# Kernel tuning notes

Hardware: AMD Instinct MI355X
Metric: run time of the kernel (lower is better)

## Reference

```python
import jax, jax.numpy as jnp
import numpy as np

B, P, E = 16, 1024, 768
HID, HEADS = 768, 12
DH = HID // HEADS  # 64
EPS = 1e-5


def setup_inputs() -> dict:
    key = jax.random.key(0)
    ks = jax.random.split(key, 4)
    return {
        "x": jax.random.normal(ks[0], (B, P, E), dtype=jnp.float32),
        "ln_weight": jnp.ones((P, E), dtype=jnp.float32),
        "ln_bias": jnp.zeros((P, E), dtype=jnp.float32),
        "qkv": jax.random.normal(ks[1], (E, 3 * HID), dtype=jnp.float32),
        "lin_w": jax.random.normal(ks[2], (HID, E), dtype=jnp.float32) * 0.02,
        "lin_b": jax.random.normal(ks[3], (E,), dtype=jnp.float32) * 0.02,
    }


def reference(x, ln_weight, ln_bias, qkv, lin_w, lin_b):
    # LayerNorm over the last TWO dims (patches, emb), per torch nn.LayerNorm((P, E))
    mean = jnp.mean(x, axis=(-2, -1), keepdims=True)
    var = jnp.var(x, axis=(-2, -1), keepdims=True)
    xn = (x - mean) / jnp.sqrt(var + EPS) * ln_weight + ln_bias

    # QKV projection: [B,P,E] @ [E,3*HID] -> [B,P,3*HID]
    proj = xn @ qkv
    # view(B,P,heads,-1) then permute -> [B,heads,P,3*DH]; chunk along last dim
    proj = proj.reshape(B, P, HEADS, 3 * DH).transpose(0, 2, 1, 3)
    q, k, v = proj[..., :DH], proj[..., DH:2 * DH], proj[..., 2 * DH:]

    # Softmax-free attention: (Q K^T) V
    atten = jnp.einsum("bhqd,bhkd->bhqk", q, k)  # [B,H,P,P]
    out = jnp.einsum("bhqk,bhkd->bhqd", atten, v)  # [B,H,P,DH]

    out = out.transpose(0, 2, 1, 3).reshape(B, P, HID)
    # dropout p=0.0 (eval) -> identity
    out = jax.nn.relu(out @ lin_w + lin_b)
    return out + x
```

## Files before the change

kernel.cpp:

```cpp
#include <hip/hip_runtime.h>
#include <hip/hip_bf16.h>
#include <cstdint>

#define BB   16
#define PP   1024
#define EE   768
#define HID  768
#define NH   12
#define DH   64
#define NPB  (PP * EE)
#define MROWS (BB * PP)

typedef __bf16 bf16_t;
typedef __bf16 bf16x8 __attribute__((ext_vector_type(8)));
typedef float  f32x4  __attribute__((ext_vector_type(4)));

__device__ __forceinline__ void gld16(const void* g, void* l) {
    __builtin_amdgcn_global_load_lds(
        (const __attribute__((address_space(1))) void*)(uintptr_t)g,
        (__attribute__((address_space(3))) void*)(uint32_t)(uintptr_t)l,
        16, 0, 0);
}

__global__ __launch_bounds__(256) void stats1_kernel(const float* __restrict__ x,
                                                     float* __restrict__ part) {
    int bid = blockIdx.x;
    int b = bid >> 6, s = bid & 63;
    const float4* xp = (const float4*)(x + (size_t)b * NPB + (size_t)s * 12288);
    float sum = 0.f, ss = 0.f;
#pragma unroll
    for (int i = 0; i < 12; ++i) {
        float4 v = xp[i * 256 + threadIdx.x];
        sum += v.x + v.y + v.z + v.w;
        ss  += v.x * v.x + v.y * v.y + v.z * v.z + v.w * v.w;
    }
#pragma unroll
    for (int off = 32; off > 0; off >>= 1) {
        sum += __shfl_down(sum, off, 64);
        ss  += __shfl_down(ss,  off, 64);
    }
    __shared__ float tmp[8];
    int wave = threadIdx.x >> 6, lane = threadIdx.x & 63;
    if (lane == 0) { tmp[wave * 2] = sum; tmp[wave * 2 + 1] = ss; }
    __syncthreads();
    if (threadIdx.x == 0) {
        part[bid * 2]     = tmp[0] + tmp[2] + tmp[4] + tmp[6];
        part[bid * 2 + 1] = tmp[1] + tmp[3] + tmp[5] + tmp[7];
    }
}

__global__ __launch_bounds__(256) void prep_kernel(const float* __restrict__ qkvw,
                                                   const float* __restrict__ linw,
                                                   const float* __restrict__ part,
                                                   bf16_t* __restrict__ qkvT,
                                                   bf16_t* __restrict__ lwT,
                                                   float* __restrict__ stats) {
    int bid = blockIdx.x;
    if (bid < 6912) {
        int idx = bid * 256 + threadIdx.x;
        int c = idx / 768, r = idx - c * 768;
        qkvT[idx] = (bf16_t)qkvw[(size_t)r * 2304 + c];
    } else if (bid < 9216) {
        int idx = (bid - 6912) * 256 + threadIdx.x;
        int c = idx / 768, r = idx - c * 768;
        lwT[idx] = (bf16_t)linw[(size_t)r * 768 + c];
    } else {
        int wave = threadIdx.x >> 6, lane = threadIdx.x & 63;
#pragma unroll
        for (int j = 0; j < 4; ++j) {
            int b = wave * 4 + j;
            float sum = part[(b * 64 + lane) * 2];
            float ss  = part[(b * 64 + lane) * 2 + 1];
#pragma unroll
            for (int off = 32; off > 0; off >>= 1) {
                sum += __shfl_down(sum, off, 64);
                ss  += __shfl_down(ss,  off, 64);
            }
            if (lane == 0) {
                const float inv_n = 1.f / (float)NPB;
                float mean = sum * inv_n;
                float var  = ss * inv_n - mean * mean;
                stats[b * 2]     = mean;
                stats[b * 2 + 1] = rsqrtf(var + 1e-5f);
            }
        }
    }
}

__global__ __launch_bounds__(256) void ln_apply_kernel(const float* __restrict__ x,
                                                       const float* __restrict__ lnw,
                                                       const float* __restrict__ lnb,
                                                       const float* __restrict__ stats,
                                                       bf16_t* __restrict__ xn) {
    int i = (blockIdx.x * 256 + threadIdx.x) * 8;
    int b = i / NPB;
    int r = i - b * NPB;
    float mean = stats[b * 2], rstd = stats[b * 2 + 1];
    float4 x0 = *(const float4*)(x + i),     x1 = *(const float4*)(x + i + 4);
    float4 w0 = *(const float4*)(lnw + r),   w1 = *(const float4*)(lnw + r + 4);
    float4 c0 = *(const float4*)(lnb + r),   c1 = *(const float4*)(lnb + r + 4);
    union { bf16_t h[8]; uint4 u; } o;
    o.h[0] = (bf16_t)((x0.x - mean) * rstd * w0.x + c0.x);
    o.h[1] = (bf16_t)((x0.y - mean) * rstd * w0.y + c0.y);
    o.h[2] = (bf16_t)((x0.z - mean) * rstd * w0.z + c0.z);
    o.h[3] = (bf16_t)((x0.w - mean) * rstd * w0.w + c0.w);
    o.h[4] = (bf16_t)((x1.x - mean) * rstd * w1.x + c1.x);
    o.h[5] = (bf16_t)((x1.y - mean) * rstd * w1.y + c1.y);
    o.h[6] = (bf16_t)((x1.z - mean) * rstd * w1.z + c1.z);
    o.h[7] = (bf16_t)((x1.w - mean) * rstd * w1.w + c1.w);
    *(uint4*)(xn + i) = o.u;
}

template <int KDIM>
__device__ __forceinline__ void gemm_core_128(const bf16_t* __restrict__ A,
                                              const bf16_t* __restrict__ Bt,
                                              int mBase, int nBase,
                                              f32x4 acc[4][4],
                                              bf16_t* As, bf16_t* Bs) {
    const int t = threadIdx.x;
    const int lane = t & 63, wave = t >> 6;
    const int wm = wave >> 1, wn = wave & 1;
    const int m16 = lane & 15, quad = lane >> 4;

    const int sr = t >> 3, s8 = t & 7;
    const bf16_t* pa[4]; const bf16_t* pb[4];
#pragma unroll
    for (int i = 0; i < 4; ++i) {
        int row = i * 32 + sr;
        int g = (s8 - (row & 7)) & 7;
        pa[i] = A  + (size_t)(mBase + row) * KDIM + g * 8;
        pb[i] = Bt + (size_t)(nBase + row) * KDIM + g * 8;
    }

    int raOff[4][2], rbOff[4][2];
#pragma unroll
    for (int i = 0; i < 4; ++i) {
        int ra = wm * 64 + i * 16 + m16;
        int rb = wn * 64 + i * 16 + m16;
#pragma unroll
        for (int ks = 0; ks < 2; ++ks) {
            raOff[i][ks] = ra * 64 + (((ks * 4 + quad) + (ra & 7)) & 7) * 8;
            rbOff[i][ks] = rb * 64 + (((ks * 4 + quad) + (rb & 7)) & 7) * 8;
        }
    }

    const f32x4 z = {0.f, 0.f, 0.f, 0.f};
#pragma unroll
    for (int mm = 0; mm < 4; ++mm)
#pragma unroll
        for (int nn = 0; nn < 4; ++nn) acc[mm][nn] = z;

    for (int k0 = 0; k0 < KDIM; k0 += 64) {
        __syncthreads();
#pragma unroll
        for (int i = 0; i < 4; ++i) {
            gld16(pa[i] + k0, As + i * 2048 + t * 8);
            gld16(pb[i] + k0, Bs + i * 2048 + t * 8);
        }
        __syncthreads();
#pragma unroll
        for (int ks = 0; ks < 2; ++ks) {
            bf16x8 af[4], bfv[4];
#pragma unroll
            for (int i = 0; i < 4; ++i) {
                af[i]  = *(const bf16x8*)(As + raOff[i][ks]);
                bfv[i] = *(const bf16x8*)(Bs + rbOff[i][ks]);
            }
#pragma unroll
            for (int mm = 0; mm < 4; ++mm)
#pragma unroll
                for (int nn = 0; nn < 4; ++nn)
                    acc[mm][nn] = __builtin_amdgcn_mfma_f32_16x16x32_bf16(
                        af[mm], bfv[nn], acc[mm][nn], 0, 0, 0);
        }
    }
}

__global__ __launch_bounds__(256) void gemm_qkv_kernel(const bf16_t* __restrict__ xn,
                                                       const bf16_t* __restrict__ qkvT,
                                                       bf16_t* __restrict__ q,
                                                       bf16_t* __restrict__ kt,
                                                       bf16_t* __restrict__ vt) {
    __shared__ bf16_t smem[16384];
    f32x4 acc[4][4];
    const int lb  = blockIdx.y * 18 + blockIdx.x;
    const int swz = (lb & 7) * 288 + (lb >> 3);
    const int tx  = swz % 18, ty = swz / 18;
    const int mBase = ty * 128, nBase = tx * 128;
    gemm_core_128<768>(xn, qkvT, mBase, nBase, acc, smem, smem + 8192);

    const int t = threadIdx.x;
    const int lane = t & 63, wave = t >> 6;
    const int wm = wave >> 1, wn = wave & 1;
    const int m16 = lane & 15, quad = lane >> 4;
    const int b = mBase >> 10, p0 = mBase & 1023;

#pragma unroll
    for (int half = 0; half < 2; ++half) {
        const int g = tx * 2 + half;
        const int cls = g % 3, h = g / 3;
        const size_t bh = (size_t)(b * NH + h);
        __syncthreads();
        if (cls == 0) {
            if (wn == half) {
#pragma unroll
                for (int mm = 0; mm < 4; ++mm)
#pragma unroll
                    for (int nn = 0; nn < 4; ++nn)
#pragma unroll
                        for (int i = 0; i < 4; ++i)
                            smem[(wm * 64 + mm * 16 + quad * 4 + i) * 72 + nn * 16 + m16] =
                                (bf16_t)acc[mm][nn][i];
            }
            __syncthreads();
#pragma unroll
            for (int it = 0; it < 4; ++it) {
                int slot = it * 256 + t;
                int r = slot >> 3, cc = slot & 7;
                bf16x8 val = *(const bf16x8*)(smem + r * 72 + cc * 8);
                *(bf16x8*)(q + ((size_t)(b * PP + p0 + r)) * HID + h * DH + cc * 8) = val;
            }
        } else {
            bf16_t* dst = (cls == 1) ? kt : vt;
            if (wn == half) {
#pragma unroll
                for (int mm = 0; mm < 4; ++mm)
#pragma unroll
                    for (int nn = 0; nn < 4; ++nn) {
                        int c = nn * 16 + m16;
                        int r0 = wm * 64 + mm * 16 + quad * 4;
                        union { bf16_t hh[4]; uint2 u; } pk;
#pragma unroll
                        for (int i = 0; i < 4; ++i) pk.hh[i] = (bf16_t)acc[mm][nn][i];
                        *(uint2*)(&smem[c * 136 + r0]) = pk.u;
                    }
            }
            __syncthreads();
#pragma unroll
            for (int it = 0; it < 4; ++it) {
                int slot = it * 256 + t;
                int d = slot >> 4, pc = slot & 15;
                bf16x8 val = *(const bf16x8*)(smem + d * 136 + pc * 8);
                *(bf16x8*)(dst + (bh * DH + d) * PP + p0 + pc * 8) = val;
            }
        }
    }
}

__global__ __launch_bounds__(256) void kv_kernel(const bf16_t* __restrict__ kt,
                                                 const bf16_t* __restrict__ vt,
                                                 bf16_t* __restrict__ thi,
                                                 bf16_t* __restrict__ tlo) {
    __shared__ float red[4 * 64 * 65];
    const int bh = blockIdx.x;
    const bf16_t* Kb = kt + (size_t)bh * DH * PP;
    const bf16_t* Vb = vt + (size_t)bh * DH * PP;
    const int t = threadIdx.x;
    const int lane = t & 63, wave = t >> 6;
    const int m16 = lane & 15, quad = lane >> 4;
    const f32x4 z = {0.f, 0.f, 0.f, 0.f};
    f32x4 acc[4][4];
#pragma unroll
    for (int mm = 0; mm < 4; ++mm)
#pragma unroll
        for (int nn = 0; nn < 4; ++nn) acc[mm][nn] = z;

    for (int ks = 0; ks < 8; ++ks) {
        int kb = wave * 256 + ks * 32 + quad * 8;
        bf16x8 af[4], bfv[4];
#pragma unroll
        for (int mm = 0; mm < 4; ++mm)
            af[mm] = *(const bf16x8*)(Kb + (size_t)(mm * 16 + m16) * PP + kb);
#pragma unroll
        for (int nn = 0; nn < 4; ++nn)
            bfv[nn] = *(const bf16x8*)(Vb + (size_t)(nn * 16 + m16) * PP + kb);
#pragma unroll
        for (int mm = 0; mm < 4; ++mm)
#pragma unroll
            for (int nn = 0; nn < 4; ++nn)
                acc[mm][nn] = __builtin_amdgcn_mfma_f32_16x16x32_bf16(
                    af[mm], bfv[nn], acc[mm][nn], 0, 0, 0);
    }
#pragma unroll
    for (int mm = 0; mm < 4; ++mm)
#pragma unroll
        for (int nn = 0; nn < 4; ++nn)
#pragma unroll
            for (int i = 0; i < 4; ++i)
                red[wave * 4160 + (mm * 16 + quad * 4 + i) * 65 + nn * 16 + m16] =
                    acc[mm][nn][i];
    __syncthreads();
#pragma unroll
    for (int j = 0; j < 16; ++j) {
        int idx = j * 256 + t;
        int m = idx >> 6, n = idx & 63;
        int a = m * 65 + n;
        float s = red[a] + red[4160 + a] + red[8320 + a] + red[12480 + a];
        bf16_t hi = (bf16_t)s;
        float lo = s - (float)hi;
        thi[(size_t)bh * 4096 + idx] = hi;
        tlo[(size_t)bh * 4096 + idx] = (bf16_t)lo;
    }
}

__global__ __launch_bounds__(256) void u_kernel(const bf16_t* __restrict__ thi,
                                                const bf16_t* __restrict__ tlo,
                                                const bf16_t* __restrict__ lwT,
                                                bf16_t* __restrict__ ut) {
    const int bh = blockIdx.x;
    const int b = bh / NH, h = bh - b * NH;
    const int nBase = blockIdx.y * 256;
    const bf16_t* Th = thi + (size_t)bh * 4096;
    const bf16_t* Tl = tlo + (size_t)bh * 4096;
    const int t = threadIdx.x, lane = t & 63, wave = t >> 6;
    const int wm = wave >> 1, wn = wave & 1;
    const int m16 = lane & 15, quad = lane >> 4;
    const f32x4 z = {0.f, 0.f, 0.f, 0.f};
    f32x4 acc[2][8];
#pragma unroll
    for (int mm = 0; mm < 2; ++mm)
#pragma unroll
        for (int nn = 0; nn < 8; ++nn) acc[mm][nn] = z;

#pragma unroll
    for (int ks = 0; ks < 2; ++ks) {
        bf16x8 ah[2], al[2], bfr[8];
#pragma unroll
        for (int mm = 0; mm < 2; ++mm) {
            ah[mm] = *(const bf16x8*)(Th + (wm * 32 + mm * 16 + m16) * 64 + ks * 32 + quad * 8);
            al[mm] = *(const bf16x8*)(Tl + (wm * 32 + mm * 16 + m16) * 64 + ks * 32 + quad * 8);
        }
#pragma unroll
        for (int nn = 0; nn < 8; ++nn)
            bfr[nn] = *(const bf16x8*)(
                lwT + (size_t)(nBase + wn * 128 + nn * 16 + m16) * 768 + h * 64 + ks * 32 + quad * 8);
#pragma unroll
        for (int mm = 0; mm < 2; ++mm)
#pragma unroll
            for (int nn = 0; nn < 8; ++nn) {
                acc[mm][nn] = __builtin_amdgcn_mfma_f32_16x16x32_bf16(
                    ah[mm], bfr[nn], acc[mm][nn], 0, 0, 0);
                acc[mm][nn] = __builtin_amdgcn_mfma_f32_16x16x32_bf16(
                    al[mm], bfr[nn], acc[mm][nn], 0, 0, 0);
            }
    }
#pragma unroll
    for (int mm = 0; mm < 2; ++mm)
#pragma unroll
        for (int nn = 0; nn < 8; ++nn) {
            int e  = nBase + wn * 128 + nn * 16 + m16;
            int d1 = wm * 32 + mm * 16 + quad * 4;
            union { bf16_t hh[4]; uint2 u; } pk;
#pragma unroll
            for (int i = 0; i < 4; ++i) pk.hh[i] = (bf16_t)acc[mm][nn][i];
            *(uint2*)(ut + ((size_t)b * 768 + e) * 768 + h * 64 + d1) = pk.u;
        }
}

__global__ __launch_bounds__(256) void gemm_out_kernel(const bf16_t* __restrict__ q,
                                                       const bf16_t* __restrict__ ut,
                                                       const float* __restrict__ linb,
                                                       const float* __restrict__ x,
                                                       float* __restrict__ out) {
    __shared__ bf16_t smem[16384];
    f32x4 acc[4][4];
    const int lb  = blockIdx.y * 6 + blockIdx.x;
    const int swz = (lb & 7) * 96 + (lb >> 3);
    const int tx  = swz % 6, ty = swz / 6;
    const int mBase = ty * 128, nBase = tx * 128;
    const int b = mBase >> 10;
    gemm_core_128<768>(q, ut + (size_t)b * 768 * 768, mBase, nBase, acc,
                       smem, smem + 8192);

    const int lane = threadIdx.x & 63, wave = threadIdx.x >> 6;
    const int wm = wave >> 1, wn = wave & 1;
    const int m16 = lane & 15, quad = lane >> 4;
#pragma unroll
    for (int mm = 0; mm < 4; ++mm) {
#pragma unroll
        for (int i = 0; i < 4; ++i) {
            size_t row = mBase + wm * 64 + mm * 16 + quad * 4 + i;
#pragma unroll
            for (int nn = 0; nn < 4; ++nn) {
                int col = nBase + wn * 64 + nn * 16 + m16;
                float v = acc[mm][nn][i] + linb[col];
                v = fmaxf(v, 0.f) + x[row * EE + col];
                out[row * EE + col] = v;
            }
        }
    }
}

extern "C" void kernel_launch(void* const* d_in, const int* in_sizes, int n_in,
                              void* d_out, int out_size, void* d_ws, size_t ws_size,
                              hipStream_t stream) {
    const float* x    = (const float*)d_in[0];
    const float* lnw  = (const float*)d_in[1];
    const float* lnb  = (const float*)d_in[2];
    const float* qkvw = (const float*)d_in[3];
    const float* linw = (const float*)d_in[4];
    const float* linb = (const float*)d_in[5];
    float* out = (float*)d_out;
    char* ws = (char*)d_ws;

    float*  part  = (float*)(ws + 0);
    float*  stats = (float*)(ws + 8192);
    bf16_t* xn    = (bf16_t*)(ws + 8448);
    bf16_t* qkvT  = (bf16_t*)(ws + 25174272);
    bf16_t* lwT   = (bf16_t*)(ws + 28713216);
    bf16_t* q     = (bf16_t*)(ws + 29892864);
    bf16_t* kt    = (bf16_t*)(ws + 55058688);
    bf16_t* vt    = (bf16_t*)(ws + 80224512);
    bf16_t* thi   = qkvT;
    bf16_t* tlo   = qkvT + 192 * 4096;
    bf16_t* ut    = kt;

    stats1_kernel<<<dim3(BB * 64), dim3(256), 0, stream>>>(x, part);
    prep_kernel<<<dim3(9217), dim3(256), 0, stream>>>(qkvw, linw, part, qkvT, lwT, stats);
    ln_apply_kernel<<<dim3(6144), dim3(256), 0, stream>>>(x, lnw, lnb, stats, xn);
    gemm_qkv_kernel<<<dim3(18, 128), dim3(256), 0, stream>>>(xn, qkvT, q, kt, vt);
    kv_kernel<<<dim3(192), dim3(256), 0, stream>>>(kt, vt, thi, tlo);
    u_kernel<<<dim3(192, 3), dim3(256), 0, stream>>>(thi, tlo, lwT, ut);
    gemm_out_kernel<<<dim3(6, 128), dim3(256), 0, stream>>>(q, ut, linb, x, out);
}
```

Baseline: 276.6 us.

## Enlarge QKV GEMM to 256x256 tiles with double-buffered LDS and tiled weight transpose

```diff
diff --git a/kernel.cpp b/kernel.cpp
--- a/kernel.cpp
+++ b/kernel.cpp
@@ -56,14 +56,37 @@
                                                    bf16_t* __restrict__ lwT,
                                                    float* __restrict__ stats) {
     int bid = blockIdx.x;
-    if (bid < 6912) {
-        int idx = bid * 256 + threadIdx.x;
-        int c = idx / 768, r = idx - c * 768;
-        qkvT[idx] = (bf16_t)qkvw[(size_t)r * 2304 + c];
-    } else if (bid < 9216) {
-        int idx = (bid - 6912) * 256 + threadIdx.x;
-        int c = idx / 768, r = idx - c * 768;
-        lwT[idx] = (bf16_t)linw[(size_t)r * 768 + c];
+    if (bid < 576) {
+        __shared__ float lds[64][65];
+        const float* src; bf16_t* dst; int r0, c0, W;
+        if (bid < 432) {
+            int tr = bid / 36, tc = bid - tr * 36;
+            r0 = tr * 64; c0 = tc * 64; src = qkvw; W = 2304; dst = qkvT;
+        } else {
+            int bb = bid - 432;
+            int tr = bb / 12, tc = bb - tr * 12;
+            r0 = tr * 64; c0 = tc * 64; src = linw; W = 768; dst = lwT;
+        }
+        int t = threadIdx.x;
+        int rr = t >> 4, cc4 = (t & 15) * 4;
+#pragma unroll
+        for (int j = 0; j < 4; ++j) {
+            float4 v = *(const float4*)(src + (size_t)(r0 + rr + j * 16) * W + c0 + cc4);
+            lds[rr + j * 16][cc4 + 0] = v.x;
+            lds[rr + j * 16][cc4 + 1] = v.y;
+            lds[rr + j * 16][cc4 + 2] = v.z;
+            lds[rr + j * 16][cc4 + 3] = v.w;
+        }
+        __syncthreads();
+        int cl = t >> 3, rgl = (t & 7) * 8;
+#pragma unroll
+        for (int jj = 0; jj < 2; ++jj) {
+            int c = jj * 32 + cl;
+            union { bf16_t h[8]; uint4 u; } o;
+#pragma unroll
+            for (int k = 0; k < 8; ++k) o.h[k] = (bf16_t)lds[rgl + k][c];
+            *(uint4*)(dst + (size_t)(c0 + c) * 768 + r0 + rgl) = o.u;
+        }
     } else {
         int wave = threadIdx.x >> 6, lane = threadIdx.x & 63;
 #pragma unroll
@@ -176,72 +199,161 @@
     }
 }
 
-__global__ __launch_bounds__(256) void gemm_qkv_kernel(const bf16_t* __restrict__ xn,
-                                                       const bf16_t* __restrict__ qkvT,
-                                                       bf16_t* __restrict__ q,
-                                                       bf16_t* __restrict__ kt,
-                                                       bf16_t* __restrict__ vt) {
-    __shared__ bf16_t smem[16384];
-    f32x4 acc[4][4];
-    const int lb  = blockIdx.y * 18 + blockIdx.x;
-    const int swz = (lb & 7) * 288 + (lb >> 3);
-    const int tx  = swz % 18, ty = swz / 18;
-    const int mBase = ty * 128, nBase = tx * 128;
-    gemm_core_128<768>(xn, qkvT, mBase, nBase, acc, smem, smem + 8192);
-
-    const int t = threadIdx.x;
-    const int lane = t & 63, wave = t >> 6;
-    const int wm = wave >> 1, wn = wave & 1;
+#define MFMA_PHASE(AF, BF, MO, NO)                                           \
+    do {                                                                     \
+        __builtin_amdgcn_s_setprio(1);                                       \
+        _Pragma("unroll") for (int mf2 = 0; mf2 < 4; ++mf2)                  \
+        _Pragma("unroll") for (int nf2 = 0; nf2 < 2; ++nf2)                  \
+        _Pragma("unroll") for (int ks2 = 0; ks2 < 2; ++ks2)                  \
+            acc[(MO) + mf2][(NO) + nf2] =                                    \
+                __builtin_amdgcn_mfma_f32_16x16x32_bf16(                     \
+                    AF[mf2][ks2], BF[nf2][ks2],                              \
+                    acc[(MO) + mf2][(NO) + nf2], 0, 0, 0);                   \
+        __builtin_amdgcn_s_setprio(0);                                       \
+    } while (0)
+
+__global__ __launch_bounds__(512, 2) void gemm_qkv_kernel(const bf16_t* __restrict__ xn,
+                                                          const bf16_t* __restrict__ qkvT,
+                                                          bf16_t* __restrict__ q,
+                                                          bf16_t* __restrict__ kt,
+                                                          bf16_t* __restrict__ vt) {
+    __shared__ bf16_t smem[65536];
+    const int t = threadIdx.x, lane = t & 63, wave = t >> 6;
+    const int wm = wave >> 2, wn = wave & 3;
     const int m16 = lane & 15, quad = lane >> 4;
+
+    const int lb = blockIdx.y * 9 + blockIdx.x;
+    const int id = (lb & 7) * 72 + (lb >> 3);
+    const int tx = id % 9, ty = id / 9;
+    const int mBase = ty * 256, nBase = tx * 256;
+
+    const int sr = t >> 3, s8 = t & 7;
+    const int g8 = (s8 - (sr & 7)) & 7;
+    const bf16_t* pa = xn   + (size_t)(mBase + sr) * 768 + g8 * 8;
+    const bf16_t* pb = qkvT + (size_t)(nBase + sr) * 768 + g8 * 8;
+
+    const int ch0 = ((quad + (m16 & 7)) & 7) * 8;
+    const int ch1 = (((4 + quad) + (m16 & 7)) & 7) * 8;
+    const int aBase = wm * 8192 + m16 * 64;
+    const int bBase = 16384 + (wn >> 1) * 8192 + ((wn & 1) * 64 + m16) * 64;
+
+    f32x4 acc[8][4];
+    const f32x4 z = {0.f, 0.f, 0.f, 0.f};
+#pragma unroll
+    for (int mm = 0; mm < 8; ++mm)
+#pragma unroll
+        for (int nn = 0; nn < 4; ++nn) acc[mm][nn] = z;
+
+#pragma unroll
+    for (int i = 0; i < 4; ++i) {
+        gld16(pa + (size_t)i * 49152, smem + i * 4096 + t * 8);
+        gld16(pb + (size_t)i * 49152, smem + 16384 + i * 4096 + t * 8);
+    }
+    __syncthreads();
+
+#pragma unroll
+    for (int ktile = 0; ktile < 12; ++ktile) {
+        const int par = (ktile & 1) << 15;
+        const int nxt = ((ktile + 1) & 1) << 15;
+        bf16x8 a0[4][2], a1[4][2], b0[2][2], b1[2][2];
+        if (ktile + 1 < 12) {
+#pragma unroll
+            for (int i = 0; i < 4; ++i) {
+                gld16(pa + (size_t)i * 49152 + (ktile + 1) * 64,
+                      smem + nxt + i * 4096 + t * 8);
+                gld16(pb + (size_t)i * 49152 + (ktile + 1) * 64,
+                      smem + nxt + 16384 + i * 4096 + t * 8);
+            }
+        }
+#pragma unroll
+        for (int mf = 0; mf < 4; ++mf) {
+            a0[mf][0] = *(const bf16x8*)(smem + par + aBase + mf * 1024 + ch0);
+            a0[mf][1] = *(const bf16x8*)(smem + par + aBase + mf * 1024 + ch1);
+        }
+#pragma unroll
+        for (int nf = 0; nf < 2; ++nf) {
+            b0[nf][0] = *(const bf16x8*)(smem + par + bBase + nf * 1024 + ch0);
+            b0[nf][1] = *(const bf16x8*)(smem + par + bBase + nf * 1024 + ch1);
+        }
+        MFMA_PHASE(a0, b0, 0, 0);
+        __builtin_amdgcn_s_barrier();
+#pragma unroll
+        for (int nf = 0; nf < 2; ++nf) {
+            b1[nf][0] = *(const bf16x8*)(smem + par + bBase + (2 + nf) * 1024 + ch0);
+            b1[nf][1] = *(const bf16x8*)(smem + par + bBase + (2 + nf) * 1024 + ch1);
+        }
+        MFMA_PHASE(a0, b1, 0, 2);
+        __builtin_amdgcn_s_barrier();
+#pragma unroll
+        for (int mf = 0; mf < 4; ++mf) {
+            a1[mf][0] = *(const bf16x8*)(smem + par + aBase + (4 + mf) * 1024 + ch0);
+            a1[mf][1] = *(const bf16x8*)(smem + par + aBase + (4 + mf) * 1024 + ch1);
+        }
+        MFMA_PHASE(a1, b0, 4, 0);
+        __builtin_amdgcn_s_barrier();
+        MFMA_PHASE(a1, b1, 4, 2);
+        __syncthreads();
+    }
+
+    bf16_t* slot = smem + wave * 8192;
+    const int g64 = tx * 4 + wn;
+    const int cls = g64 % 3, h = g64 / 3;
     const int b = mBase >> 10, p0 = mBase & 1023;
-
-#pragma unroll
-    for (int half = 0; half < 2; ++half) {
-        const int g = tx * 2 + half;
-        const int cls = g % 3, h = g / 3;
-        const size_t bh = (size_t)(b * NH + h);
-        __syncthreads();
-        if (cls == 0) {
-            if (wn == half) {
-#pragma unroll
-                for (int mm = 0; mm < 4; ++mm)
-#pragma unroll
-                    for (int nn = 0; nn < 4; ++nn)
-#pragma unroll
-                        for (int i = 0; i < 4; ++i)
-                            smem[(wm * 64 + mm * 16 + quad * 4 + i) * 72 + nn * 16 + m16] =
-                                (bf16_t)acc[mm][nn][i];
-            }
-            __syncthreads();
-#pragma unroll
-            for (int it = 0; it < 4; ++it) {
-                int slot = it * 256 + t;
-                int r = slot >> 3, cc = slot & 7;
-                bf16x8 val = *(const bf16x8*)(smem + r * 72 + cc * 8);
-                *(bf16x8*)(q + ((size_t)(b * PP + p0 + r)) * HID + h * DH + cc * 8) = val;
-            }
-        } else {
-            bf16_t* dst = (cls == 1) ? kt : vt;
-            if (wn == half) {
-#pragma unroll
-                for (int mm = 0; mm < 4; ++mm)
-#pragma unroll
-                    for (int nn = 0; nn < 4; ++nn) {
-                        int c = nn * 16 + m16;
-                        int r0 = wm * 64 + mm * 16 + quad * 4;
-                        union { bf16_t hh[4]; uint2 u; } pk;
-#pragma unroll
-                        for (int i = 0; i < 4; ++i) pk.hh[i] = (bf16_t)acc[mm][nn][i];
-                        *(uint2*)(&smem[c * 136 + r0]) = pk.u;
-                    }
-            }
-            __syncthreads();
-#pragma unroll
-            for (int it = 0; it < 4; ++it) {
-                int slot = it * 256 + t;
-                int d = slot >> 4, pc = slot & 15;
-                bf16x8 val = *(const bf16x8*)(smem + d * 136 + pc * 8);
-                *(bf16x8*)(dst + (bh * DH + d) * PP + p0 + pc * 8) = val;
+    const int rowTile = p0 + wm * 128;
+
+    if (cls == 0) {
+#pragma unroll
+        for (int pass = 0; pass < 2; ++pass) {
+#pragma unroll
+            for (int mf2 = 0; mf2 < 4; ++mf2)
+#pragma unroll
+                for (int nf = 0; nf < 4; ++nf)
+#pragma unroll
+                    for (int i = 0; i < 4; ++i)
+                        slot[(mf2 * 16 + quad * 4 + i) * 72 + nf * 16 + m16] =
+                            (bf16_t)acc[pass * 4 + mf2][nf][i];
+            asm volatile("s_waitcnt lgkmcnt(0)" ::: "memory");
+            __builtin_amdgcn_sched_barrier(0);
+#pragma unroll
+            for (int j = 0; j < 8; ++j) {
+                int r = j * 8 + (lane >> 3), cc = lane & 7;
+                bf16x8 val = *(const bf16x8*)(slot + r * 72 + cc * 8);
+                *(bf16x8*)(q + ((size_t)(b * 1024 + rowTile + pass * 64 + r)) * 768 +
+                           h * 64 + cc * 8) = val;
+            }
+            if (pass == 0) {
+                asm volatile("s_waitcnt lgkmcnt(0)" ::: "memory");
+                __builtin_amdgcn_sched_barrier(0);
+            }
+        }
+    } else {
+        bf16_t* dst = (cls == 1) ? kt : vt;
+        const size_t bh = (size_t)(b * 12 + h);
+#pragma unroll
+        for (int pass = 0; pass < 2; ++pass) {
+#pragma unroll
+            for (int mf2 = 0; mf2 < 4; ++mf2)
+#pragma unroll
+                for (int nf = 0; nf < 4; ++nf) {
+                    int c = nf * 16 + m16;
+                    union { bf16_t hh[4]; uint2 u; } pk;
+#pragma unroll
+                    for (int i = 0; i < 4; ++i)
+                        pk.hh[i] = (bf16_t)acc[pass * 4 + mf2][nf][i];
+                    *(uint2*)(slot + c * 72 + mf2 * 16 + quad * 4) = pk.u;
+                }
+            asm volatile("s_waitcnt lgkmcnt(0)" ::: "memory");
+            __builtin_amdgcn_sched_barrier(0);
+#pragma unroll
+            for (int j = 0; j < 8; ++j) {
+                int c = (lane >> 3) + j * 8, r8 = (lane & 7) * 8;
+                bf16x8 val = *(const bf16x8*)(slot + c * 72 + r8);
+                *(bf16x8*)(dst + (bh * 64 + c) * 1024 + p0 + wm * 128 +
+                           pass * 64 + r8) = val;
+            }
+            if (pass == 0) {
+                asm volatile("s_waitcnt lgkmcnt(0)" ::: "memory");
+                __builtin_amdgcn_sched_barrier(0);
             }
         }
     }
@@ -416,9 +528,9 @@
     bf16_t* ut    = kt;
 
     stats1_kernel<<<dim3(BB * 64), dim3(256), 0, stream>>>(x, part);
-    prep_kernel<<<dim3(9217), dim3(256), 0, stream>>>(qkvw, linw, part, qkvT, lwT, stats);
+    prep_kernel<<<dim3(577), dim3(256), 0, stream>>>(qkvw, linw, part, qkvT, lwT, stats);
     ln_apply_kernel<<<dim3(6144), dim3(256), 0, stream>>>(x, lnw, lnb, stats, xn);
-    gemm_qkv_kernel<<<dim3(18, 128), dim3(256), 0, stream>>>(xn, qkvT, q, kt, vt);
+    gemm_qkv_kernel<<<dim3(9, 64), dim3(512), 0, stream>>>(xn, qkvT, q, kt, vt);
     kv_kernel<<<dim3(192), dim3(256), 0, stream>>>(kt, vt, thi, tlo);
     u_kernel<<<dim3(192, 3), dim3(256), 0, stream>>>(thi, tlo, lwT, ut);
     gemm_out_kernel<<<dim3(6, 128), dim3(256), 0, stream>>>(q, ut, linb, x, out);
```

Result: faster. 260.5 us (-5.8%).
